# Kernel tuning notes

Hardware: AMD Instinct MI355X
Metric: run time of the kernel (lower is better)

The kernel has to match this reference:

```python
import jax, jax.numpy as jnp
import numpy as np

FEATURE_DIM = 128

def setup_inputs() -> dict:
    key0 = jax.random.key(0)
    k1, k2, k3 = jax.random.split(key0, 3)
    B, NQ, NK, D = 4, 4096, 4096, FEATURE_DIM
    return {
        "target": jax.random.normal(k1, (B, NQ, D), dtype=jnp.float32),
        "key": jax.random.normal(k2, (B, NK, D), dtype=jnp.float32),
        "value": jax.random.normal(k3, (B, NK, D), dtype=jnp.float32),
    }

def reference(target, key, value):
    # Lan_K F: scores = target @ key^T / sqrt(d); weights = softmax(scores); out = weights @ value
    scale = 1.0 / np.sqrt(FEATURE_DIM).astype(np.float32)
    scores = jnp.einsum('bqd,bkd->bqk', target, key) * scale  # [B, NQ, NK]
    weights = jax.nn.softmax(scores, axis=-1)
    return jnp.einsum('bqk,bkd->bqd', weights, value)  # [B, NQ, D]
```

## Files before the change

kernel.cpp:

```cpp
#include <hip/hip_runtime.h>
#include <stdint.h>

#define B_ 4
#define NQ_ 4096
#define NK_ 4096
#define D_ 128
#define BM_ 64
#define BN_ 128
#define NITER_ (NK_/BN_)
#define KVBUF_ 33792
#define PS_ 136
#define OS_ 66

typedef __attribute__((ext_vector_type(8))) short short8;
typedef __attribute__((ext_vector_type(4))) float floatx4;
typedef unsigned int u32;

union frag_u { u32 u[4]; short8 s; };
union pair_u { u32 u[2]; uint2 v; };

__device__ __forceinline__ unsigned short f2bf_rne(float x){
  union { float f; u32 u; } c; c.f = x;
  u32 u = c.u;
  return (unsigned short)((u + 0x7fffu + ((u >> 16) & 1u)) >> 16);
}
__device__ __forceinline__ u32 pk2bf(float a, float b){
  union { float f; u32 u; } x, y; x.f = a; y.f = b;
  return ((x.u + 0x8000u) >> 16) | ((y.u + 0x8000u) & 0xffff0000u);
}

#define GLD16(gp, lp) __builtin_amdgcn_global_load_lds( \
    (const __attribute__((address_space(1))) u32*)(gp),  \
    (__attribute__((address_space(3))) u32*)(lp), 16, 0, 0)

#define TS_ 136
__global__ void prep_kernel(const float* __restrict__ k, const float* __restrict__ v,
                            unsigned short* __restrict__ kb, unsigned short* __restrict__ vt){
  if (blockIdx.x >= 256){
    int base = (blockIdx.x - 256) * 2048 + threadIdx.x;
    #pragma unroll
    for (int i = 0; i < 8; i++){
      int j = base + i*256;
      float4 val = ((const float4*)k)[j];
      ushort4 s;
      s.x = f2bf_rne(val.x); s.y = f2bf_rne(val.y);
      s.z = f2bf_rne(val.z); s.w = f2bf_rne(val.w);
      ((ushort4*)kb)[j] = s;
    }
    return;
  }
  __shared__ __align__(16) float tile[64*TS_];
  int blk = blockIdx.x; int b = blk >> 6; int kt = blk & 63; int k0 = kt*64;
  int t = threadIdx.x;
  const float* vb = v + ((size_t)b*NK_ + k0)*D_;
  #pragma unroll
  for (int i=0;i<8;i++){
    int f = t + i*256;
    int row = f >> 5, c4 = f & 31;
    *(float4*)(tile + row*TS_ + c4*4) = *(const float4*)(vb + row*D_ + c4*4);
  }
  __syncthreads();
  unsigned short* vtb = vt + (size_t)b*D_*NK_ + k0;
  #pragma unroll
  for (int i=0;i<16;i++){
    int u2 = t + i*256;
    int d = u2 >> 5, kp = u2 & 31;
    ushort2 s2;
    s2.x = f2bf_rne(tile[(2*kp)*TS_ + d]);
    s2.y = f2bf_rne(tile[(2*kp+1)*TS_ + d]);
    *(ushort2*)(vtb + (size_t)d*NK_ + 2*kp) = s2;
  }
}

__global__ __launch_bounds__(512, 2) void attn_kernel(
    const float* __restrict__ Qf, const unsigned short* __restrict__ Kb,
    const unsigned short* __restrict__ Vt, float* __restrict__ Out){
  __shared__ __align__(16) char sm[154624];
  char* smKb = sm;
  char* smVb = sm + 2*KVBUF_;
  unsigned short* smP = (unsigned short*)(sm + 4*KVBUF_);
  float* smL = (float*)(sm + 4*KVBUF_ + 64*PS_*2);
  float* smO = (float*)sm;

  const int bi = blockIdx.x;
  const int b  = (bi >> 1) & 3;
  const int qt = ((bi >> 3) << 1) | (bi & 1);
  const int q0 = qt * BM_;
  const int tid = threadIdx.x;
  const int w = tid >> 6, lane = tid & 63;
  const int kg = w >> 1, dh = w & 1;
  const int l15 = lane & 15, l4 = lane >> 4;

  const unsigned short* kgb = Kb + (size_t)b * NK_ * D_;
  const unsigned short* vgb = Vt + (size_t)b * D_ * NK_;

  #pragma unroll
  for (int i = 0; i < 4; i++){
    int c = w*4 + i;
    { int kgc = c>>3, cp = c&7;
      int dchunk = kgc*8 + (cp&1)*4 + (cp>>1);
      const unsigned short* g = kgb + (size_t)(kgc*32 + cp*4 + (lane>>4))*D_ + (lane&15)*8;
      GLD16(g, smKb + dchunk*1056); }
    { const unsigned short* g = vgb + (size_t)(c*4 + (lane>>4))*NK_ + (lane&15)*8;
      GLD16(g, smVb + c*1056); }
  }

  short8 qf[4][4];
  {
    const float* qp = Qf + ((size_t)b*NQ_ + q0)*D_;
    #pragma unroll
    for (int nb = 0; nb < 4; nb++)
      #pragma unroll
      for (int kb = 0; kb < 4; kb++){
        const float* p = qp + (size_t)(nb*16 + l15)*D_ + kb*32 + l4*8;
        float4 a = *(const float4*)p;
        float4 c4 = *(const float4*)(p + 4);
        frag_u f;
        f.u[0] = pk2bf(a.x, a.y);  f.u[1] = pk2bf(a.z, a.w);
        f.u[2] = pk2bf(c4.x, c4.y); f.u[3] = pk2bf(c4.z, c4.w);
        qf[nb][kb] = f.s;
      }
  }

  floatx4 o[4][4];
  #pragma unroll
  for (int nb = 0; nb < 4; nb++)
    #pragma unroll
    for (int dt = 0; dt < 4; dt++) o[nb][dt] = (floatx4)0.0f;
  float lsum[4] = {0.f, 0.f, 0.f, 0.f};

  const float SL = 0.08838834764831845f * 1.4426950408889634f;

  __syncthreads();

  for (int it = 0; it < NITER_; ++it){
    const int buf = it & 1;
    char* kcur = smKb + buf * KVBUF_;
    char* vcur = smVb + buf * KVBUF_;

    if (it + 1 < NITER_){
      char* knxt = smKb + (buf ^ 1) * KVBUF_;
      #pragma unroll
      for (int i = 0; i < 4; i++){
        int c = w*4 + i;
        int kgc = c>>3, cp = c&7;
        int dchunk = kgc*8 + (cp&1)*4 + (cp>>1);
        const unsigned short* g = kgb + (size_t)((it+1)*BN_ + kgc*32 + cp*4 + (lane>>4))*D_ + (lane&15)*8;
        GLD16(g, knxt + dchunk*1056);
      }
    }

    short8 kf[4];
    {
      int row = kg*32 + dh*16 + l15;
      char* base = kcur + (row>>2)*1056 + (row&3)*256 + l4*16;
      kf[0] = *(const short8*)(base);
      kf[1] = *(const short8*)(base + 64);
      kf[2] = *(const short8*)(base + 128);
      kf[3] = *(const short8*)(base + 192);
    }
    floatx4 s[4];
    #pragma unroll
    for (int nb = 0; nb < 4; nb++){
      s[nb] = (floatx4)0.0f;
      s[nb] = __builtin_amdgcn_mfma_f32_16x16x32_bf16(kf[0], qf[nb][0], s[nb], 0,0,0);
      s[nb] = __builtin_amdgcn_mfma_f32_16x16x32_bf16(kf[1], qf[nb][1], s[nb], 0,0,0);
      s[nb] = __builtin_amdgcn_mfma_f32_16x16x32_bf16(kf[2], qf[nb][2], s[nb], 0,0,0);
      s[nb] = __builtin_amdgcn_mfma_f32_16x16x32_bf16(kf[3], qf[nb][3], s[nb], 0,0,0);
    }

    #pragma unroll
    for (int nb = 0; nb < 4; nb++){
      float p0 = __builtin_amdgcn_exp2f(s[nb][0] * SL);
      float p1 = __builtin_amdgcn_exp2f(s[nb][1] * SL);
      float p2 = __builtin_amdgcn_exp2f(s[nb][2] * SL);
      float p3 = __builtin_amdgcn_exp2f(s[nb][3] * SL);
      lsum[nb] += (p0 + p1) + (p2 + p3);
      pair_u pp; pp.u[0] = pk2bf(p0, p1); pp.u[1] = pk2bf(p2, p3);
      *(uint2*)(smP + (size_t)(nb*16 + l15)*PS_ + kg*32 + l4*8 + dh*4) = pp.v;
    }

    __syncthreads();

    if (it + 1 < NITER_){
      char* vnxt = smVb + (buf ^ 1) * KVBUF_;
      #pragma unroll
      for (int i = 0; i < 4; i++){
        int c = w*4 + i;
        const unsigned short* g = vgb + (size_t)(c*4 + (lane>>4))*NK_ + (it+1)*BN_ + (lane&15)*8;
        GLD16(g, vnxt + c*1056);
      }
    }

    short8 pf[4];
    #pragma unroll
    for (int nb = 0; nb < 4; nb++)
      pf[nb] = *(const short8*)(smP + (size_t)(nb*16 + l15)*PS_ + kg*32 + l4*8);
    short8 vf[4];
    #pragma unroll
    for (int dt = 0; dt < 4; dt++){
      int d = dh*64 + dt*16 + l15;
      vf[dt] = *(const short8*)(vcur + (d>>2)*1056 + (d&3)*256 + (kg*32 + l4*8)*2);
    }
    #pragma unroll
    for (int nb = 0; nb < 4; nb++)
      #pragma unroll
      for (int dt = 0; dt < 4; dt++)
        o[nb][dt] = __builtin_amdgcn_mfma_f32_16x16x32_bf16(pf[nb], vf[dt], o[nb][dt], 0,0,0);

    __syncthreads();
  }

  #pragma unroll
  for (int nb = 0; nb < 4; nb++){
    float v = lsum[nb];
    v += __shfl_xor(v, 16);
    v += __shfl_xor(v, 32);
    lsum[nb] = v;
  }
  if (l4 == 0)
    #pragma unroll
    for (int nb = 0; nb < 4; nb++)
      smL[w*64 + nb*16 + l15] = lsum[nb];

  if (w >= 4){
    float* r = smO + (size_t)(w - 4) * 4224;
    #pragma unroll
    for (int nb = 0; nb < 4; nb++)
      #pragma unroll
      for (int dt = 0; dt < 4; dt++)
        #pragma unroll
        for (int q = 0; q < 4; q++)
          r[(size_t)(nb*16 + l4*4 + q)*OS_ + dt*16 + l15] = o[nb][dt][q];
  }
  __syncthreads();
  if (w < 4){
    float* r = smO + (size_t)w * 4224;
    #pragma unroll
    for (int nb = 0; nb < 4; nb++)
      #pragma unroll
      for (int dt = 0; dt < 4; dt++)
        #pragma unroll
        for (int q = 0; q < 4; q++)
          o[nb][dt][q] += r[(size_t)(nb*16 + l4*4 + q)*OS_ + dt*16 + l15];
  }
  __syncthreads();
  if (w == 2 || w == 3){
    float* r = smO + (size_t)(w - 2) * 4224;
    #pragma unroll
    for (int nb = 0; nb < 4; nb++)
      #pragma unroll
      for (int dt = 0; dt < 4; dt++)
        #pragma unroll
        for (int q = 0; q < 4; q++)
          r[(size_t)(nb*16 + l4*4 + q)*OS_ + dt*16 + l15] = o[nb][dt][q];
  }
  __syncthreads();
  if (w < 2){
    float* r = smO + (size_t)w * 4224;
    float* og = Out + ((size_t)b*NQ_ + q0)*D_ + dh*64;
    #pragma unroll
    for (int nb = 0; nb < 4; nb++)
      #pragma unroll
      for (int q = 0; q < 4; q++){
        int row = nb*16 + l4*4 + q;
        float lt = 0.f;
        #pragma unroll
        for (int w2 = 0; w2 < 8; w2++) lt += smL[w2*64 + row];
        float inv = 1.0f / lt;
        #pragma unroll
        for (int dt = 0; dt < 4; dt++){
          float val = o[nb][dt][q] + r[(size_t)row*OS_ + dt*16 + l15];
          og[(size_t)row*D_ + dt*16 + l15] = val * inv;
        }
      }
  }
}

extern "C" void kernel_launch(void* const* d_in, const int* in_sizes, int n_in,
                              void* d_out, int out_size, void* d_ws, size_t ws_size,
                              hipStream_t stream){
  const float* q = (const float*)d_in[0];
  const float* k = (const float*)d_in[1];
  const float* v = (const float*)d_in[2];
  float* out = (float*)d_out;
  unsigned short* kb = (unsigned short*)d_ws;
  unsigned short* vt = kb + (size_t)B_*NK_*D_;
  prep_kernel<<<512, 256, 0, stream>>>(k, v, kb, vt);
  attn_kernel<<<256, 512, 0, stream>>>(q, kb, vt, out);
}
```

Baseline: 131.6 us.

## Load K and V fragments directly from global into registers, double-buffer P

New measurement: 141.5 us. 7.5% more time.

```diff
diff --git a/kernel.cpp b/kernel.cpp
--- a/kernel.cpp
+++ b/kernel.cpp
@@ -8,7 +8,6 @@
 #define BM_ 64
 #define BN_ 128
 #define NITER_ (NK_/BN_)
-#define KVBUF_ 33792
 #define PS_ 136
 #define OS_ 66
 
@@ -28,10 +27,6 @@
   union { float f; u32 u; } x, y; x.f = a; y.f = b;
   return ((x.u + 0x8000u) >> 16) | ((y.u + 0x8000u) & 0xffff0000u);
 }
-
-#define GLD16(gp, lp) __builtin_amdgcn_global_load_lds( \
-    (const __attribute__((address_space(1))) u32*)(gp),  \
-    (__attribute__((address_space(3))) u32*)(lp), 16, 0, 0)
 
 #define TS_ 136
 __global__ void prep_kernel(const float* __restrict__ k, const float* __restrict__ v,
@@ -75,12 +70,10 @@
 __global__ __launch_bounds__(512, 2) void attn_kernel(
     const float* __restrict__ Qf, const unsigned short* __restrict__ Kb,
     const unsigned short* __restrict__ Vt, float* __restrict__ Out){
-  __shared__ __align__(16) char sm[154624];
-  char* smKb = sm;
-  char* smVb = sm + 2*KVBUF_;
-  unsigned short* smP = (unsigned short*)(sm + 4*KVBUF_);
-  float* smL = (float*)(sm + 4*KVBUF_ + 64*PS_*2);
+  __shared__ __align__(16) char sm[69632];
+  unsigned short* smP = (unsigned short*)sm;
   float* smO = (float*)sm;
+  float* smL = (float*)(sm + 67584);
 
   const int bi = blockIdx.x;
   const int b  = (bi >> 1) & 3;
@@ -94,16 +87,13 @@
   const unsigned short* kgb = Kb + (size_t)b * NK_ * D_;
   const unsigned short* vgb = Vt + (size_t)b * D_ * NK_;
 
-  #pragma unroll
-  for (int i = 0; i < 4; i++){
-    int c = w*4 + i;
-    { int kgc = c>>3, cp = c&7;
-      int dchunk = kgc*8 + (cp&1)*4 + (cp>>1);
-      const unsigned short* g = kgb + (size_t)(kgc*32 + cp*4 + (lane>>4))*D_ + (lane&15)*8;
-      GLD16(g, smKb + dchunk*1056); }
-    { const unsigned short* g = vgb + (size_t)(c*4 + (lane>>4))*NK_ + (lane&15)*8;
-      GLD16(g, smVb + c*1056); }
-  }
+  const unsigned short* kRow =
+      kgb + (size_t)(kg*32 + (l15>>2)*8 + dh*4 + (l15&3)) * D_ + l4*8;
+  const unsigned short* vBase = vgb + kg*32 + l4*8;
+
+  short8 kf[4], knf[4];
+  #pragma unroll
+  for (int j = 0; j < 4; j++) kf[j] = *(const short8*)(kRow + j*32);
 
   short8 qf[4][4];
   {
@@ -131,34 +121,20 @@
 
   const float SL = 0.08838834764831845f * 1.4426950408889634f;
 
-  __syncthreads();
-
   for (int it = 0; it < NITER_; ++it){
-    const int buf = it & 1;
-    char* kcur = smKb + buf * KVBUF_;
-    char* vcur = smVb + buf * KVBUF_;
-
+    short8 vf[4];
+    const unsigned short* vit = vBase + (size_t)it * BN_;
+    #pragma unroll
+    for (int dt = 0; dt < 4; dt++){
+      int d = dh*64 + dt*16 + l15;
+      vf[dt] = *(const short8*)(vit + (size_t)d * NK_);
+    }
     if (it + 1 < NITER_){
-      char* knxt = smKb + (buf ^ 1) * KVBUF_;
-      #pragma unroll
-      for (int i = 0; i < 4; i++){
-        int c = w*4 + i;
-        int kgc = c>>3, cp = c&7;
-        int dchunk = kgc*8 + (cp&1)*4 + (cp>>1);
-        const unsigned short* g = kgb + (size_t)((it+1)*BN_ + kgc*32 + cp*4 + (lane>>4))*D_ + (lane&15)*8;
-        GLD16(g, knxt + dchunk*1056);
-      }
-    }
-
-    short8 kf[4];
-    {
-      int row = kg*32 + dh*16 + l15;
-      char* base = kcur + (row>>2)*1056 + (row&3)*256 + l4*16;
-      kf[0] = *(const short8*)(base);
-      kf[1] = *(const short8*)(base + 64);
-      kf[2] = *(const short8*)(base + 128);
-      kf[3] = *(const short8*)(base + 192);
-    }
+      const unsigned short* kp = kRow + (size_t)(it+1) * (BN_ * D_);
+      #pragma unroll
+      for (int j = 0; j < 4; j++) knf[j] = *(const short8*)(kp + j*32);
+    }
+
     floatx4 s[4];
     #pragma unroll
     for (int nb = 0; nb < 4; nb++){
@@ -169,6 +145,7 @@
       s[nb] = __builtin_amdgcn_mfma_f32_16x16x32_bf16(kf[3], qf[nb][3], s[nb], 0,0,0);
     }
 
+    unsigned short* smPb = smP + (it & 1) * (64 * PS_);
     #pragma unroll
     for (int nb = 0; nb < 4; nb++){
       float p0 = __builtin_amdgcn_exp2f(s[nb][0] * SL);
@@ -177,38 +154,23 @@
       float p3 = __builtin_amdgcn_exp2f(s[nb][3] * SL);
       lsum[nb] += (p0 + p1) + (p2 + p3);
       pair_u pp; pp.u[0] = pk2bf(p0, p1); pp.u[1] = pk2bf(p2, p3);
-      *(uint2*)(smP + (size_t)(nb*16 + l15)*PS_ + kg*32 + l4*8 + dh*4) = pp.v;
+      *(uint2*)(smPb + (size_t)(nb*16 + l15)*PS_ + kg*32 + l4*8 + dh*4) = pp.v;
     }
 
     __syncthreads();
 
-    if (it + 1 < NITER_){
-      char* vnxt = smVb + (buf ^ 1) * KVBUF_;
-      #pragma unroll
-      for (int i = 0; i < 4; i++){
-        int c = w*4 + i;
-        const unsigned short* g = vgb + (size_t)(c*4 + (lane>>4))*NK_ + (it+1)*BN_ + (lane&15)*8;
-        GLD16(g, vnxt + c*1056);
-      }
-    }
-
     short8 pf[4];
     #pragma unroll
     for (int nb = 0; nb < 4; nb++)
-      pf[nb] = *(const short8*)(smP + (size_t)(nb*16 + l15)*PS_ + kg*32 + l4*8);
-    short8 vf[4];
-    #pragma unroll
-    for (int dt = 0; dt < 4; dt++){
-      int d = dh*64 + dt*16 + l15;
-      vf[dt] = *(const short8*)(vcur + (d>>2)*1056 + (d&3)*256 + (kg*32 + l4*8)*2);
-    }
+      pf[nb] = *(const short8*)(smPb + (size_t)(nb*16 + l15)*PS_ + kg*32 + l4*8);
     #pragma unroll
     for (int nb = 0; nb < 4; nb++)
       #pragma unroll
       for (int dt = 0; dt < 4; dt++)
         o[nb][dt] = __builtin_amdgcn_mfma_f32_16x16x32_bf16(pf[nb], vf[dt], o[nb][dt], 0,0,0);
 
-    __syncthreads();
+    #pragma unroll
+    for (int j = 0; j < 4; j++) kf[j] = knf[j];
   }
 
   #pragma unroll
@@ -222,6 +184,8 @@
     #pragma unroll
     for (int nb = 0; nb < 4; nb++)
       smL[w*64 + nb*16 + l15] = lsum[nb];
+
+  __syncthreads();
 
   if (w >= 4){
     float* r = smO + (size_t)(w - 4) * 4224;
```
